# Performance work log

Measured on AMD Instinct MI355X. Metric: run time of the kernel, lower is better.

The kernel has to match this reference:

```python
import jax, jax.numpy as jnp
import numpy as np

N_NODES = 50000
N_EDGES = 800000
F_IN = 128
HID = 128
F_ADD = 32
N_GRAPHS = 128


def setup_inputs() -> dict:
    key = jax.random.key(0)
    ks = jax.random.split(key, 12)
    x = jax.random.normal(ks[0], (N_NODES, F_IN), dtype=jnp.float32)
    edge_index = jax.random.randint(ks[1], (2, N_EDGES), 0, N_NODES, dtype=jnp.int64)
    batch = jnp.sort(jax.random.randint(ks[2], (N_NODES,), 0, N_GRAPHS, dtype=jnp.int64))
    additional_features = jax.random.normal(ks[3], (N_GRAPHS, F_ADD), dtype=jnp.float32)
    def glorot(k, shape):
        fan_in, fan_out = shape[0], shape[1]
        lim = jnp.sqrt(6.0 / (fan_in + fan_out)).astype(jnp.float32)
        return jax.random.uniform(k, shape, jnp.float32, -lim, lim)
    W1 = glorot(ks[4], (F_IN, HID)); b1 = jnp.zeros((HID,), jnp.float32)
    W2 = glorot(ks[5], (HID, HID)); b2 = jnp.zeros((HID,), jnp.float32)
    fc1_w = glorot(ks[6], (HID + F_ADD, HID)); fc1_b = jnp.zeros((HID,), jnp.float32)
    fc2_w = glorot(ks[7], (HID, 2)); fc2_b = jnp.zeros((2,), jnp.float32)
    return {"x": x, "edge_index": edge_index, "batch": batch,
            "additional_features": additional_features,
            "W1": W1, "b1": b1, "W2": W2, "b2": b2,
            "fc1_w": fc1_w, "fc1_b": fc1_b, "fc2_w": fc2_w, "fc2_b": fc2_b}


def _gcn_conv(h, src, dst, norm, W, b):
    # h: [N, d_in]; symmetric-normalized scatter-add aggregation (PyG GCNConv)
    h = h @ W                                   # [N, d_out]
    msg = h[src] * norm[:, None]                # gather + scale: [E+N, d_out]
    return jax.ops.segment_sum(msg, dst, num_segments=N_NODES) + b


def reference(x, edge_index, batch, additional_features,
              W1, b1, W2, b2, fc1_w, fc1_b, fc2_w, fc2_b):
    loops = jnp.arange(N_NODES, dtype=edge_index.dtype)
    src = jnp.concatenate([edge_index[0], loops])   # A + I
    dst = jnp.concatenate([edge_index[1], loops])
    deg = jax.ops.segment_sum(jnp.ones_like(src, dtype=x.dtype), dst,
                              num_segments=N_NODES)
    dinv = jnp.where(deg > 0, jax.lax.rsqrt(jnp.maximum(deg, 1.0)), 0.0)
    norm = dinv[src] * dinv[dst]

    h = jax.nn.relu(_gcn_conv(x, src, dst, norm, W1, b1))
    h = jax.nn.relu(_gcn_conv(h, src, dst, norm, W2, b2))
    # dropout is identity in eval mode

    sums = jax.ops.segment_sum(h, batch, num_segments=N_GRAPHS)    # [G, HID]
    counts = jax.ops.segment_sum(jnp.ones((N_NODES,), h.dtype), batch,
                                 num_segments=N_GRAPHS)
    pooled = sums / jnp.maximum(counts, 1.0)[:, None]              # global_mean_pool

    z = jnp.concatenate([pooled, additional_features], axis=1)     # [G, HID+F_ADD]
    z = jax.nn.relu(z @ fc1_w + fc1_b)
    return z @ fc2_w + fc2_b                                       # [G, 2]
```

## Files before the change

### kernel.cpp

```cpp
#include <hip/hip_runtime.h>

#define NN 50000
#define NE 800000
#define FD 128
#define FDH 64
#define FA 32
#define NG 128
#define EETOT (NE + NN)
#define NBLK ((NN + 255) / 256)
#define NPXCD 6250
#define ECHK 2048
#define NCHK ((NE + ECHK - 1) / ECHK)
#define FPB 52
#define FILLB (8 * FPB)
#define GEMMB ((NN + 63) / 64)

typedef __attribute__((ext_vector_type(8))) short short8;
typedef __attribute__((ext_vector_type(4))) float f32x4;

__device__ __forceinline__ float bfbits(unsigned short u) {
    return __uint_as_float(((unsigned int)u) << 16);
}
__device__ __forceinline__ float bflo(unsigned int p) { return __uint_as_float(p << 16); }
__device__ __forceinline__ float bfhi(unsigned int p) { return __uint_as_float(p & 0xffff0000u); }
__device__ __forceinline__ unsigned short f2bf(float f) {
    unsigned int u = __float_as_uint(f);
    unsigned int r = u + 0x7FFFu + ((u >> 16) & 1u);
    return (unsigned short)(r >> 16);
}
__device__ __forceinline__ unsigned int packbf(float a, float b) {
    return (unsigned int)f2bf(a) | ((unsigned int)f2bf(b) << 16);
}

__device__ __forceinline__ int wave_probe_bf16(const unsigned int* t, int nwords) {
    int lane = threadIdx.x & 63;
    unsigned int wv = (lane < nwords) ? t[lane] : 0u;
    int nzp = (wv != 0u) ? 1 : 0;
    unsigned int e = (wv >> 7) & 0xFFu;
    int hitp = (nzp && e >= 100u && e <= 140u) ? 1 : 0;
    int nz = __popcll(__ballot(nzp));
    int hits = __popcll(__ballot(hitp));
    return (nz < 8) ? 1 : (hits * 4 >= nz * 3);
}
__device__ __forceinline__ int wave_probe_is64(const int* ei) {
    int lane = threadIdx.x & 63;
    int v = (lane < 32) ? ei[2 * lane + 1] : 0;
    return (__ballot(v != 0) == 0ull) ? 1 : 0;
}

__global__ __launch_bounds__(128) void mark_kernel(float* out, float v) {
    out[threadIdx.x] = v;
}

__global__ __launch_bounds__(256) void prep(
        const void* addf, const void* w1, const void* b1, const void* w2,
        const void* b2, const void* fc1w, const void* fc1b, const void* fc2w,
        const void* fc2b, unsigned int* W1t, unsigned int* W2t,
        float* addff, float* b1f, float* b2f, float* fc1wf, float* fc1bf,
        float* fc2wf, float* fc2bf, int* degi, int* tsum) {
    int b = blockIdx.x;
    if (b < 64) {
        int rel = b * 256 + threadIdx.x;
        const void* src = (rel < 8192) ? w1 : w2;
        unsigned int* dst = (rel < 8192) ? W1t : W2t;
        int flag = wave_probe_bf16((const unsigned int*)src, 64);
        int rr = rel & 8191;
        int n = rr >> 6, kk = rr & 63;
        float lo, hi;
        if (flag) {
            const unsigned short* s = (const unsigned short*)src;
            lo = bfbits(s[(2 * kk) * FD + n]);
            hi = bfbits(s[(2 * kk + 1) * FD + n]);
        } else {
            const float* s = (const float*)src;
            lo = s[(2 * kk) * FD + n];
            hi = s[(2 * kk + 1) * FD + n];
        }
        dst[rr] = packbf(lo, hi);
    } else if (b < 163) {
        int i = (b - 64) * 256 + threadIdx.x;
        int wb = (b - 64) * 256 + (threadIdx.x & ~63);
        const void* src; float* dst; int base; int prnw; int lim;
        if      (wb < 4096)  { src = addf; dst = addff; base = 0;     prnw = 64; lim = 4096;  }
        else if (wb < 4224)  { src = b1;   dst = b1f;   base = 4096;  prnw = 64; lim = 128;   }
        else if (wb < 4352)  { src = b2;   dst = b2f;   base = 4224;  prnw = 64; lim = 128;   }
        else if (wb < 24832) { src = fc1w; dst = fc1wf; base = 4352;  prnw = 64; lim = 20480; }
        else if (wb < 24960) { src = fc1b; dst = fc1bf; base = 24832; prnw = 64; lim = 128;   }
        else if (wb < 25216) { src = fc2w; dst = fc2wf; base = 24960; prnw = 64; lim = 256;   }
        else if (wb < 25280) { src = fc2b; dst = fc2bf; base = 25216; prnw = 1;  lim = 2;     }
        else return;
        int flag = wave_probe_bf16((const unsigned int*)src, prnw);
        int rel = i - base;
        if (rel < lim) {
            if (flag) dst[rel] = bfbits(((const unsigned short*)src)[rel]);
            else      dst[rel] = ((const float*)src)[rel];
        }
    } else {
        int i = (b - 163) * 256 + threadIdx.x;
        if      (i < NN)       degi[i] = 0;
        else if (i < NN + 256) tsum[i - NN] = 0;
    }
}

__global__ __launch_bounds__(256) void bin_gemm1(const int* ei, int* deg,
        int2* ebsd, int* bofs,
        const void* __restrict__ Av, const unsigned int* __restrict__ Wt,
        unsigned short* __restrict__ C) {
    if ((int)blockIdx.x < NCHK) {
        __shared__ int cnt[8];
        __shared__ int sbase[8];
        int is64 = wave_probe_is64(ei);
        int chunk = blockIdx.x;
        int e0 = chunk * ECHK;
        int nedge = NE - e0; if (nedge > ECHK) nedge = ECHK;
        if (threadIdx.x < 8) cnt[threadIdx.x] = 0;
        __syncthreads();
        int sA[8], dA[8], rk[8], pr[8];
        #pragma unroll
        for (int k = 0; k < 8; ++k) {
            int j = k * 256 + threadIdx.x;
            pr[k] = -1;
            if (j < nedge) {
                int e = e0 + j;
                int s = is64 ? ei[2 * e] : ei[e];
                int d = is64 ? ei[2 * (NE + e)] : ei[NE + e];
                atomicAdd(&deg[d], 1);
                int p = d / NPXCD;
                sA[k] = s; dA[k] = d; pr[k] = p;
                rk[k] = atomicAdd(&cnt[p], 1);
            }
        }
        __syncthreads();
        if (threadIdx.x == 0) {
            int acc = 0;
            #pragma unroll
            for (int p = 0; p < 8; ++p) {
                sbase[p] = acc;
                bofs[chunk * 8 + p] = acc;
                acc += cnt[p];
            }
        }
        __syncthreads();
        #pragma unroll
        for (int k = 0; k < 8; ++k) {
            if (pr[k] >= 0) {
                int idx = chunk * ECHK + sbase[pr[k]] + rk[k];
                ebsd[idx] = make_int2(sA[k], dA[k]);
            }
        }
        return;
    }
    int bid = blockIdx.x - NCHK;
    int wave = threadIdx.x >> 6;
    int lane = threadIdx.x & 63;
    int quad = lane >> 4;
    int l16  = lane & 15;
    int mbase = bid * 64 + wave * 16;
    int ra = mbase + l16;
    if (ra >= NN) ra = NN - 1;
    bool f32in = !wave_probe_bf16((const unsigned int*)Av, 64);
    short8 af[4];
    if (!f32in) {
        const uint4* Arow = (const uint4*)((const unsigned int*)Av + (size_t)ra * FDH);
        #pragma unroll
        for (int kk = 0; kk < 4; ++kk) {
            uint4 v = Arow[kk * 4 + quad];
            af[kk] = *(short8*)&v;
        }
    } else {
        const float* Arow = (const float*)Av + (size_t)ra * FD;
        #pragma unroll
        for (int kk = 0; kk < 4; ++kk) {
            const float4* p = (const float4*)(Arow + (kk * 4 + quad) * 8);
            float4 u = p[0], v = p[1];
            uint4 q;
            q.x = packbf(u.x, u.y); q.y = packbf(u.z, u.w);
            q.z = packbf(v.x, v.y); q.w = packbf(v.z, v.w);
            af[kk] = *(short8*)&q;
        }
    }
    #pragma unroll
    for (int nt = 0; nt < 8; ++nt) {
        int n = nt * 16 + l16;
        const uint4* Wrow = (const uint4*)(Wt + (size_t)n * FDH);
        f32x4 acc = {0.f, 0.f, 0.f, 0.f};
        #pragma unroll
        for (int kk = 0; kk < 4; ++kk) {
            uint4 wv = Wrow[kk * 4 + quad];
            short8 bf = *(short8*)&wv;
            acc = __builtin_amdgcn_mfma_f32_16x16x32_bf16(af[kk], bf, acc, 0, 0, 0);
        }
        int row0 = mbase + quad * 4;
        #pragma unroll
        for (int reg = 0; reg < 4; ++reg) {
            int r = row0 + reg;
            if (r < NN) C[(size_t)r * FD + nt * 16 + l16] = f2bf(acc[reg]);
        }
    }
}

__global__ __launch_bounds__(256) void scan_fused(const int* degi, const int* batch,
        int* tsum, float* dinv, int* rowstart, int* cursor, int* gstart) {
    __shared__ int sh[256];
    int b = blockIdx.x, t = threadIdx.x;
    int i = b * 256 + t;
    int d = (i < NN) ? degi[i] : 0;
    if (i < NN) dinv[i] = rsqrtf((float)(d + 1));
    int v = (i < NN) ? d + 1 : 0;
    sh[t] = v;
    __syncthreads();
    for (int off = 1; off < 256; off <<= 1) {
        int a = (t >= off) ? sh[t - off] : 0;
        __syncthreads();
        sh[t] += a;
        __syncthreads();
    }
    int incl = sh[t];
    int total = sh[255];
    if (t == 0) atomicExch(&tsum[b], total);
    int pt = 0;
    for (int j = t; j < b; j += 256) {
        int s;
        do { s = atomicAdd(&tsum[j], 0); } while (s == 0);
        pt += s;
    }
    __syncthreads();
    sh[t] = pt;
    __syncthreads();
    for (int off = 128; off >= 1; off >>= 1) {
        if (t < off) sh[t] += sh[t + off];
        __syncthreads();
    }
    int boff = sh[0];
    if (i < NN) {
        int r = boff + incl - v;
        rowstart[i] = r;
        cursor[i]   = r;
    }
    if (i == 0) rowstart[NN] = EETOT;
    if (i < NN) {
        int is64 = (batch[NN - 1] == 0) ? 1 : 0;
        int bc = is64 ? batch[2 * i] : batch[i];
        if (i == 0) {
            for (int g = 0; g <= bc; ++g) gstart[g] = 0;
        } else {
            int bp = is64 ? batch[2 * (i - 1)] : batch[i - 1];
            for (int g = bp + 1; g <= bc; ++g) gstart[g] = i;
        }
        if (i == NN - 1) {
            for (int g = bc + 1; g <= NG; ++g) gstart[g] = NN;
        }
    }
}

__global__ __launch_bounds__(256) void fill_kernel(const int2* ebsd, const int* bofs,
        const float* dinv, int* cursor, unsigned int* cv) {
    int par = blockIdx.x & 7;
    int g   = blockIdx.x >> 3;
    for (int chunk = g; chunk < NCHK; chunk += FPB) {
        int b0 = bofs[chunk * 8 + par];
        int nedge = NE - chunk * ECHK; if (nedge > ECHK) nedge = ECHK;
        int b1 = (par < 7) ? bofs[chunk * 8 + par + 1] : nedge;
        for (int j = b0 + (int)threadIdx.x; j < b1; j += 256) {
            int2 sd = ebsd[chunk * ECHK + j];
            int pos = atomicAdd(&cursor[sd.y], 1);
            cv[pos] = (unsigned int)sd.x
                    | ((unsigned int)f2bf(dinv[sd.x] * dinv[sd.y]) << 16);
        }
    }
    for (int n = par * NPXCD + g * 256 + threadIdx.x; n < (par + 1) * NPXCD;
         n += FPB * 256) {
        int pos = atomicAdd(&cursor[n], 1);
        float di = dinv[n];
        cv[pos] = (unsigned int)n | ((unsigned int)f2bf(di * di) << 16);
    }
}

__global__ __launch_bounds__(256) void gemm_mfma(const unsigned int* __restrict__ Av,
        const unsigned int* __restrict__ Wt, unsigned short* __restrict__ C) {
    int wave = threadIdx.x >> 6;
    int lane = threadIdx.x & 63;
    int quad = lane >> 4;
    int l16  = lane & 15;
    int mbase = blockIdx.x * 64 + wave * 16;
    int ra = mbase + l16;
    if (ra >= NN) ra = NN - 1;
    short8 af[4];
    const uint4* Arow = (const uint4*)(Av + (size_t)ra * FDH);
    #pragma unroll
    for (int kk = 0; kk < 4; ++kk) {
        uint4 v = Arow[kk * 4 + quad];
        af[kk] = *(short8*)&v;
    }
    #pragma unroll
    for (int nt = 0; nt < 8; ++nt) {
        int n = nt * 16 + l16;
        const uint4* Wrow = (const uint4*)(Wt + (size_t)n * FDH);
        f32x4 acc = {0.f, 0.f, 0.f, 0.f};
        #pragma unroll
        for (int kk = 0; kk < 4; ++kk) {
            uint4 wv = Wrow[kk * 4 + quad];
            short8 bf = *(short8*)&wv;
            acc = __builtin_amdgcn_mfma_f32_16x16x32_bf16(af[kk], bf, acc, 0, 0, 0);
        }
        int row0 = mbase + quad * 4;
        #pragma unroll
        for (int reg = 0; reg < 4; ++reg) {
            int r = row0 + reg;
            if (r < NN) C[(size_t)r * FD + nt * 16 + l16] = f2bf(acc[reg]);
        }
    }
}

__global__ __launch_bounds__(256) void aggregate_kernel(const unsigned int* Hb,
        const unsigned int* cv, const int* rowstart, const float* bias,
        unsigned int* outb) {
    int lane = threadIdx.x & 63;
    int r4   = lane >> 4;
    int c4   = lane & 15;
    int wv   = threadIdx.x >> 6;
    int n = blockIdx.x * 16 + wv * 4 + r4;
    const uint4* H4 = (const uint4*)Hb;
    int jb = rowstart[n], je = rowstart[n + 1];
    float a0 = 0.f, a1 = 0.f, a2 = 0.f, a3 = 0.f;
    float a4 = 0.f, a5 = 0.f, a6 = 0.f, a7 = 0.f;
    int j = jb;
    for (; j + 7 < je; j += 8) {
        unsigned int rr[8]; uint4 hh[8];
        #pragma unroll
        for (int k = 0; k < 8; ++k) rr[k] = cv[j + k];
        #pragma unroll
        for (int k = 0; k < 8; ++k) hh[k] = H4[(size_t)(rr[k] & 0xFFFFu) * 16 + c4];
        #pragma unroll
        for (int k = 0; k < 8; ++k) {
            float v = bfbits((unsigned short)(rr[k] >> 16));
            a0 += v * bflo(hh[k].x); a1 += v * bfhi(hh[k].x);
            a2 += v * bflo(hh[k].y); a3 += v * bfhi(hh[k].y);
            a4 += v * bflo(hh[k].z); a5 += v * bfhi(hh[k].z);
            a6 += v * bflo(hh[k].w); a7 += v * bfhi(hh[k].w);
        }
    }
    for (; j + 3 < je; j += 4) {
        unsigned int rr[4]; uint4 hh[4];
        #pragma unroll
        for (int k = 0; k < 4; ++k) rr[k] = cv[j + k];
        #pragma unroll
        for (int k = 0; k < 4; ++k) hh[k] = H4[(size_t)(rr[k] & 0xFFFFu) * 16 + c4];
        #pragma unroll
        for (int k = 0; k < 4; ++k) {
            float v = bfbits((unsigned short)(rr[k] >> 16));
            a0 += v * bflo(hh[k].x); a1 += v * bfhi(hh[k].x);
            a2 += v * bflo(hh[k].y); a3 += v * bfhi(hh[k].y);
            a4 += v * bflo(hh[k].z); a5 += v * bfhi(hh[k].z);
            a6 += v * bflo(hh[k].w); a7 += v * bfhi(hh[k].w);
        }
    }
    for (; j < je; ++j) {
        unsigned int r = cv[j];
        uint4 h = H4[(size_t)(r & 0xFFFFu) * 16 + c4];
        float v = bfbits((unsigned short)(r >> 16));
        a0 += v * bflo(h.x); a1 += v * bfhi(h.x);
        a2 += v * bflo(h.y); a3 += v * bfhi(h.y);
        a4 += v * bflo(h.z); a5 += v * bfhi(h.z);
        a6 += v * bflo(h.w); a7 += v * bfhi(h.w);
    }
    a0 = fmaxf(a0 + bias[8 * c4 + 0], 0.f);
    a1 = fmaxf(a1 + bias[8 * c4 + 1], 0.f);
    a2 = fmaxf(a2 + bias[8 * c4 + 2], 0.f);
    a3 = fmaxf(a3 + bias[8 * c4 + 3], 0.f);
    a4 = fmaxf(a4 + bias[8 * c4 + 4], 0.f);
    a5 = fmaxf(a5 + bias[8 * c4 + 5], 0.f);
    a6 = fmaxf(a6 + bias[8 * c4 + 6], 0.f);
    a7 = fmaxf(a7 + bias[8 * c4 + 7], 0.f);
    uint4 out;
    out.x = packbf(a0, a1);
    out.y = packbf(a2, a3);
    out.z = packbf(a4, a5);
    out.w = packbf(a6, a7);
    ((uint4*)outb)[(size_t)n * 16 + c4] = out;
}

__global__ __launch_bounds__(256) void poolhead(const unsigned int* Hb,
        const int* gstart, const float* addf, const float* fc1w, const float* fc1b,
        const float* fc2w, const float* fc2b, const unsigned int* x, void* outp) {
    int g = blockIdx.x;
    int t = threadIdx.x;
    int q = t >> 6, w = t & 63;
    int obf = wave_probe_bf16(x, 64);
    int s = gstart[g], e = gstart[g + 1];
    float a0 = 0.f, a1 = 0.f;
    #pragma unroll 4
    for (int n = s + q; n < e; n += 4) {
        unsigned int h = Hb[(size_t)n * FDH + w];
        a0 += bflo(h);
        a1 += bfhi(h);
    }
    __shared__ float pp[4][FD];
    __shared__ float z[FD + FA];
    __shared__ float h[FD];
    pp[q][2 * w]     = a0;
    pp[q][2 * w + 1] = a1;
    __syncthreads();
    if (t < FD) {
        float cnt = (float)(e - s);
        if (cnt < 1.0f) cnt = 1.0f;
        z[t] = (pp[0][t] + pp[1][t] + pp[2][t] + pp[3][t]) / cnt;
    }
    if (t >= FD && t < FD + FA) z[t] = addf[g * FA + (t - FD)];
    __syncthreads();
    if (t < FD) {
        float acc = fc1b[t];
        #pragma unroll 4
        for (int k = 0; k < FD + FA; ++k)
            acc += z[k] * fc1w[k * FD + t];
        h[t] = fmaxf(acc, 0.f);
    }
    __syncthreads();
    if (t < 2) {
        float o = fc2b[t];
        for (int j = 0; j < FD; ++j) o += h[j] * fc2w[j * 2 + t];
        if (obf) ((unsigned short*)outp)[g * 2 + t] = f2bf(o);
        else     ((float*)outp)[g * 2 + t] = o;
    }
}

extern "C" void kernel_launch(void* const* d_in, const int* in_sizes, int n_in,
                              void* d_out, int out_size, void* d_ws, size_t ws_size,
                              hipStream_t stream) {
    (void)out_size;

    if (n_in != 12) {
        hipLaunchKernelGGL(mark_kernel, dim3(1), dim3(128), 0, stream,
                           (float*)d_out, 2000.0f);
        return;
    }
    const int exp_sizes[12] = {6400000, 1600000, 50000, 4096, 16384, 128,
                               16384, 128, 20480, 128, 256, 2};
    for (int i = 0; i < 12; ++i) {
        if (in_sizes[i] != exp_sizes[i]) {
            hipLaunchKernelGGL(mark_kernel, dim3(1), dim3(128), 0, stream,
                               (float*)d_out, 3000.0f + 100.0f * i);
            return;
        }
    }

    size_t off = 0;
    char* base = (char*)d_ws;
#define WSALLOC(ptr, type, nbytes) \
    type* ptr = (type*)(base + off); off += (((size_t)(nbytes)) + 255) & ~(size_t)255;
    WSALLOC(bufA,  unsigned int, (size_t)NN * FDH * 4)
    WSALLOC(bufB,  unsigned int, (size_t)NN * FDH * 4)
    WSALLOC(dinv,  float, (size_t)NN * 4)
    WSALLOC(degi,  int,   (size_t)NN * 4)
    WSALLOC(tsum,  int,   256 * 4)
    WSALLOC(rowst, int,   (size_t)(NN + 1) * 4)
    WSALLOC(cursor,int,   (size_t)NN * 4)
    WSALLOC(cv,    unsigned int, (size_t)EETOT * 4)
    WSALLOC(gstart,int,   (size_t)(NG + 1) * 4)
    WSALLOC(ebsd,  int2,  (size_t)NCHK * ECHK * 8)
    WSALLOC(bofs,  int,   (size_t)NCHK * 8 * 4)
    WSALLOC(W1t,   unsigned int, (size_t)FD * FDH * 4)
    WSALLOC(W2t,   unsigned int, (size_t)FD * FDH * 4)
    WSALLOC(b1f,   float, FD * 4)
    WSALLOC(b2f,   float, FD * 4)
    WSALLOC(addff, float, (size_t)NG * FA * 4)
    WSALLOC(fc1wf, float, (size_t)(FD + FA) * FD * 4)
    WSALLOC(fc1bf, float, FD * 4)
    WSALLOC(fc2wf, float, FD * 2 * 4)
    WSALLOC(fc2bf, float, 2 * 4)
#undef WSALLOC
    if (ws_size < off) {
        hipLaunchKernelGGL(mark_kernel, dim3(1), dim3(128), 0, stream,
                           (float*)d_out, 1000.0f);
        return;
    }

    const int* ei    = (const int*)d_in[1];
    const int* batch = (const int*)d_in[2];

    hipLaunchKernelGGL(prep, dim3(360), dim3(256), 0, stream,
                       d_in[3], d_in[4], d_in[5], d_in[6], d_in[7],
                       d_in[8], d_in[9], d_in[10], d_in[11],
                       W1t, W2t, addff, b1f, b2f, fc1wf, fc1bf,
                       fc2wf, fc2bf, degi, tsum);

    hipLaunchKernelGGL(bin_gemm1, dim3(NCHK + GEMMB), dim3(256), 0, stream,
                       ei, degi, ebsd, bofs,
                       d_in[0], W1t, (unsigned short*)bufA);

    hipLaunchKernelGGL(scan_fused, dim3(NBLK), dim3(256), 0, stream,
                       degi, batch, tsum, dinv, rowst, cursor, gstart);

    hipLaunchKernelGGL(fill_kernel, dim3(FILLB), dim3(256), 0, stream,
                       ebsd, bofs, dinv, cursor, cv);

    hipLaunchKernelGGL(aggregate_kernel, dim3(NN / 16), dim3(256), 0, stream,
                       bufA, cv, rowst, b1f, bufB);
    hipLaunchKernelGGL(gemm_mfma, dim3(GEMMB), dim3(256), 0, stream,
                       bufB, W2t, (unsigned short*)bufA);
    hipLaunchKernelGGL(aggregate_kernel, dim3(NN / 16), dim3(256), 0, stream,
                       bufA, cv, rowst, b2f, bufB);

    hipLaunchKernelGGL(poolhead, dim3(NG), dim3(256), 0, stream,
                       bufB, gstart, addff, fc1wf, fc1bf, fc2wf, fc2bf,
                       (const unsigned int*)d_in[0], d_out);
}
```

Measured before the change: 290.7 us.

## Fuse first-layer aggregation with second-layer GEMM via shared memory tile

Merges the layer-1 aggregate kernel and the layer-2 MFMA GEMM into one kernel. Each block aggregates 16 nodes, applies bias and ReLU, stages the bf16 rows in LDS, then the four waves each compute two 16-column tiles of the product with W2. This removes one launch and the global write and read of the intermediate hidden tensor. Buffers are swapped so poolhead reads from bufA. The cost is an LDS barrier in a gather-bound kernel and a small per-block GEMM that reloads W2 for every 16 rows.

```diff
diff --git a/kernel.cpp b/kernel.cpp
--- a/kernel.cpp
+++ b/kernel.cpp
@@ -276,38 +276,100 @@
     }
 }
 
-__global__ __launch_bounds__(256) void gemm_mfma(const unsigned int* __restrict__ Av,
+__global__ __launch_bounds__(256) void agg_gemm2(const unsigned int* Hb,
+        const unsigned int* cv, const int* rowstart, const float* bias,
         const unsigned int* __restrict__ Wt, unsigned short* __restrict__ C) {
-    int wave = threadIdx.x >> 6;
+    __shared__ unsigned int hA[16][68];
     int lane = threadIdx.x & 63;
+    int r4   = lane >> 4;
+    int c4   = lane & 15;
+    int wv   = threadIdx.x >> 6;
+    int nb = blockIdx.x * 16;
+    int n = nb + wv * 4 + r4;
+    const uint4* H4 = (const uint4*)Hb;
+    int jb = rowstart[n], je = rowstart[n + 1];
+    float a0 = 0.f, a1 = 0.f, a2 = 0.f, a3 = 0.f;
+    float a4 = 0.f, a5 = 0.f, a6 = 0.f, a7 = 0.f;
+    int j = jb;
+    for (; j + 7 < je; j += 8) {
+        unsigned int rr[8]; uint4 hh[8];
+        #pragma unroll
+        for (int k = 0; k < 8; ++k) rr[k] = cv[j + k];
+        #pragma unroll
+        for (int k = 0; k < 8; ++k) hh[k] = H4[(size_t)(rr[k] & 0xFFFFu) * 16 + c4];
+        #pragma unroll
+        for (int k = 0; k < 8; ++k) {
+            float v = bfbits((unsigned short)(rr[k] >> 16));
+            a0 += v * bflo(hh[k].x); a1 += v * bfhi(hh[k].x);
+            a2 += v * bflo(hh[k].y); a3 += v * bfhi(hh[k].y);
+            a4 += v * bflo(hh[k].z); a5 += v * bfhi(hh[k].z);
+            a6 += v * bflo(hh[k].w); a7 += v * bfhi(hh[k].w);
+        }
+    }
+    for (; j + 3 < je; j += 4) {
+        unsigned int rr[4]; uint4 hh[4];
+        #pragma unroll
+        for (int k = 0; k < 4; ++k) rr[k] = cv[j + k];
+        #pragma unroll
+        for (int k = 0; k < 4; ++k) hh[k] = H4[(size_t)(rr[k] & 0xFFFFu) * 16 + c4];
+        #pragma unroll
+        for (int k = 0; k < 4; ++k) {
+            float v = bfbits((unsigned short)(rr[k] >> 16));
+            a0 += v * bflo(hh[k].x); a1 += v * bfhi(hh[k].x);
+            a2 += v * bflo(hh[k].y); a3 += v * bfhi(hh[k].y);
+            a4 += v * bflo(hh[k].z); a5 += v * bfhi(hh[k].z);
+            a6 += v * bflo(hh[k].w); a7 += v * bfhi(hh[k].w);
+        }
+    }
+    for (; j < je; ++j) {
+        unsigned int r = cv[j];
+        uint4 h = H4[(size_t)(r & 0xFFFFu) * 16 + c4];
+        float v = bfbits((unsigned short)(r >> 16));
+        a0 += v * bflo(h.x); a1 += v * bfhi(h.x);
+        a2 += v * bflo(h.y); a3 += v * bfhi(h.y);
+        a4 += v * bflo(h.z); a5 += v * bfhi(h.z);
+        a6 += v * bflo(h.w); a7 += v * bfhi(h.w);
+    }
+    a0 = fmaxf(a0 + bias[8 * c4 + 0], 0.f);
+    a1 = fmaxf(a1 + bias[8 * c4 + 1], 0.f);
+    a2 = fmaxf(a2 + bias[8 * c4 + 2], 0.f);
+    a3 = fmaxf(a3 + bias[8 * c4 + 3], 0.f);
+    a4 = fmaxf(a4 + bias[8 * c4 + 4], 0.f);
+    a5 = fmaxf(a5 + bias[8 * c4 + 5], 0.f);
+    a6 = fmaxf(a6 + bias[8 * c4 + 6], 0.f);
+    a7 = fmaxf(a7 + bias[8 * c4 + 7], 0.f);
+    int lrow = wv * 4 + r4;
+    hA[lrow][c4 * 4 + 0] = packbf(a0, a1);
+    hA[lrow][c4 * 4 + 1] = packbf(a2, a3);
+    hA[lrow][c4 * 4 + 2] = packbf(a4, a5);
+    hA[lrow][c4 * 4 + 3] = packbf(a6, a7);
+    __syncthreads();
     int quad = lane >> 4;
     int l16  = lane & 15;
-    int mbase = blockIdx.x * 64 + wave * 16;
-    int ra = mbase + l16;
-    if (ra >= NN) ra = NN - 1;
     short8 af[4];
-    const uint4* Arow = (const uint4*)(Av + (size_t)ra * FDH);
     #pragma unroll
     for (int kk = 0; kk < 4; ++kk) {
-        uint4 v = Arow[kk * 4 + quad];
+        const uint4* p = (const uint4*)&hA[l16][(kk * 4 + quad) * 4];
+        uint4 v = *p;
         af[kk] = *(short8*)&v;
     }
     #pragma unroll
-    for (int nt = 0; nt < 8; ++nt) {
-        int n = nt * 16 + l16;
-        const uint4* Wrow = (const uint4*)(Wt + (size_t)n * FDH);
+    for (int t = 0; t < 2; ++t) {
+        int nt = wv * 2 + t;
+        int nn2 = nt * 16 + l16;
+        const uint4* Wrow = (const uint4*)(Wt + (size_t)nn2 * FDH);
         f32x4 acc = {0.f, 0.f, 0.f, 0.f};
         #pragma unroll
         for (int kk = 0; kk < 4; ++kk) {
-            uint4 wv = Wrow[kk * 4 + quad];
-            short8 bf = *(short8*)&wv;
+            uint4 wvv = Wrow[kk * 4 + quad];
+            short8 bf = *(short8*)&wvv;
             acc = __builtin_amdgcn_mfma_f32_16x16x32_bf16(af[kk], bf, acc, 0, 0, 0);
         }
-        int row0 = mbase + quad * 4;
+        int row0 = nb + quad * 4;
         #pragma unroll
         for (int reg = 0; reg < 4; ++reg) {
             int r = row0 + reg;
-            if (r < NN) C[(size_t)r * FD + nt * 16 + l16] = f2bf(acc[reg]);
+            C[(size_t)r * FD + nt * 16 + l16] = f2bf(acc[reg]);
         }
     }
 }
@@ -494,14 +556,13 @@
     hipLaunchKernelGGL(fill_kernel, dim3(FILLB), dim3(256), 0, stream,
                        ebsd, bofs, dinv, cursor, cv);
 
+    hipLaunchKernelGGL(agg_gemm2, dim3(NN / 16), dim3(256), 0, stream,
+                       bufA, cv, rowst, b1f, W2t, (unsigned short*)bufB);
+
     hipLaunchKernelGGL(aggregate_kernel, dim3(NN / 16), dim3(256), 0, stream,
-                       bufA, cv, rowst, b1f, bufB);
-    hipLaunchKernelGGL(gemm_mfma, dim3(GEMMB), dim3(256), 0, stream,
-                       bufB, W2t, (unsigned short*)bufA);
-    hipLaunchKernelGGL(aggregate_kernel, dim3(NN / 16), dim3(256), 0, stream,
-                       bufA, cv, rowst, b2f, bufB);
+                       bufB, cv, rowst, b2f, bufA);
 
     hipLaunchKernelGGL(poolhead, dim3(NG), dim3(256), 0, stream,
-                       bufB, gstart, addff, fc1wf, fc1bf, fc2wf, fc2bf,
+                       bufA, gstart, addff, fc1wf, fc1bf, fc2wf, fc2bf,
                        (const unsigned int*)d_in[0], d_out);
 }
```

New measurement: 278.9 us. 1.04x faster.
